# Performance work log

Hardware: AMD Instinct MI355X
Metric: run time of the kernel (lower is better)

The kernel has to match this reference:

```python
import jax, jax.numpy as jnp
import numpy as np

N_NODES = 100000
N_EDGES = 3200000
D = 64          # in == hidden == out channels
EDGE_DIM = 8
N_LAYERS = 3
EPS = 1e-5


def setup_inputs() -> dict:
    key = jax.random.key(0)
    ks = jax.random.split(key, 12)
    x = jax.random.normal(ks[0], (N_NODES, D), dtype=jnp.float32)
    edge_index = jax.random.randint(ks[1], (2, N_EDGES), 0, N_NODES, dtype=jnp.int64)
    edge_attr = jax.random.normal(ks[2], (N_EDGES, EDGE_DIM), dtype=jnp.float32)
    # per-layer HydroConv params (stacked over layers)
    lin_w = jax.random.normal(ks[3], (N_LAYERS, D, D), dtype=jnp.float32) * 0.1
    lin_b = jax.random.normal(ks[4], (N_LAYERS, D), dtype=jnp.float32) * 0.1
    emlp_w = jax.random.normal(ks[5], (N_LAYERS, 1, EDGE_DIM), dtype=jnp.float32) * 0.1
    emlp_b = jax.random.normal(ks[6], (N_LAYERS, 1), dtype=jnp.float32) * 0.1
    # per-layer LayerNorm affine params
    gamma = jnp.ones((N_LAYERS, D), dtype=jnp.float32)
    beta = jnp.zeros((N_LAYERS, D), dtype=jnp.float32)
    fc_w = jax.random.normal(ks[7], (D, D), dtype=jnp.float32) * 0.1
    fc_b = jax.random.normal(ks[8], (D,), dtype=jnp.float32) * 0.1
    return dict(x=x, edge_index=edge_index, edge_attr=edge_attr,
                lin_w=lin_w, lin_b=lin_b, emlp_w=emlp_w, emlp_b=emlp_b,
                gamma=gamma, beta=beta, fc_w=fc_w, fc_b=fc_b)


def _layer_norm(h, g, b):
    mu = jnp.mean(h, axis=-1, keepdims=True)
    var = jnp.var(h, axis=-1, keepdims=True)
    return (h - mu) * jax.lax.rsqrt(var + EPS) * g + b


def reference(x, edge_index, edge_attr, lin_w, lin_b, emlp_w, emlp_b, gamma, beta, fc_w, fc_b):
    src = edge_index[0]  # x_j (source / neighbor)
    dst = edge_index[1]  # x_i (target, aggregation index)
    h = x
    for l in range(N_LAYERS):
        identity = h
        # edge MLP: Linear(edge_dim -> 1) + Softplus  -> per-edge weight [E, 1]
        w = jax.nn.softplus(edge_attr @ emlp_w[l].T + emlp_b[l])
        # message = w * (x_j - x_i); scatter-add to targets
        msg = w * (h[src] - h[dst])                               # [E, D]
        agg = jax.ops.segment_sum(msg, dst, num_segments=N_NODES)  # [N, D]
        h = agg @ lin_w[l].T + lin_b[l]
        h = jax.nn.relu(h)
        h = _layer_norm(h, gamma[l], beta[l])
        h = h + identity  # residual (shapes always match: in == hidden)
    return h @ fc_w.T + fc_b
```

## Files before the change

### kernel.cpp

```cpp
#include <hip/hip_runtime.h>

#define NN 100000
#define NE 3200000
#define NCHUNK 98

__device__ inline unsigned short f2bf(float f) {
    unsigned int u = __float_as_uint(f);
    u += 0x7FFFu + ((u >> 16) & 1u);
    return (unsigned short)(u >> 16);
}
__device__ inline float bflo(unsigned int v) { return __uint_as_float(v << 16); }
__device__ inline float bfhi(unsigned int v) { return __uint_as_float(v & 0xFFFF0000u); }

__global__ __launch_bounds__(256) void k_transpose(
    const float* __restrict__ linw, const float* __restrict__ fcw,
    float* __restrict__ wt)
{
    const float* src = (blockIdx.x < 3) ? (linw + blockIdx.x * 4096) : fcw;
    float* dst = wt + blockIdx.x * 4096;
    for (int i = threadIdx.x; i < 4096; i += 256)
        dst[(i & 63) * 64 + (i >> 6)] = src[i];
}

__global__ __launch_bounds__(256) void k_cvt(
    const float* __restrict__ x, unsigned short* __restrict__ hb)
{
    int stride = gridDim.x * blockDim.x;
    const float4* x4 = (const float4*)x;
    ushort4* hb4 = (ushort4*)hb;
    for (int i = blockIdx.x * blockDim.x + threadIdx.x; i < NN * 16; i += stride) {
        float4 v = x4[i];
        hb4[i] = make_ushort4(f2bf(v.x), f2bf(v.y), f2bf(v.z), f2bf(v.w));
    }
}

__global__ __launch_bounds__(256) void k_hist(
    const int* __restrict__ ei, int* __restrict__ deg)
{
    int stride = gridDim.x * blockDim.x;
    for (int e = blockIdx.x * blockDim.x + threadIdx.x; e < NE; e += stride)
        atomicAdd(&deg[ei[NE + e]], 1);
}

__global__ __launch_bounds__(256) void k_scan1(
    const int* __restrict__ deg, int* __restrict__ base, int* __restrict__ csum)
{
    __shared__ int lds[256];
    int tid = threadIdx.x;
    int i0 = blockIdx.x * 1024 + tid * 4;
    int d[4];
    #pragma unroll
    for (int k = 0; k < 4; ++k) d[k] = (i0 + k < NN) ? deg[i0 + k] : 0;
    int s = d[0] + d[1] + d[2] + d[3];
    lds[tid] = s;
    __syncthreads();
    for (int off = 1; off < 256; off <<= 1) {
        int add = (tid >= off) ? lds[tid - off] : 0;
        __syncthreads();
        lds[tid] += add;
        __syncthreads();
    }
    int excl = lds[tid] - s;
    if (i0 + 0 < NN) base[i0 + 0] = excl;
    if (i0 + 1 < NN) base[i0 + 1] = excl + d[0];
    if (i0 + 2 < NN) base[i0 + 2] = excl + d[0] + d[1];
    if (i0 + 3 < NN) base[i0 + 3] = excl + d[0] + d[1] + d[2];
    if (tid == 255) csum[blockIdx.x] = lds[255];
}

__global__ __launch_bounds__(128) void k_scan2(
    const int* __restrict__ csum, int* __restrict__ coff)
{
    __shared__ int lds[128];
    int tid = threadIdx.x;
    int v = (tid < NCHUNK) ? csum[tid] : 0;
    lds[tid] = v;
    __syncthreads();
    for (int off = 1; off < 128; off <<= 1) {
        int add = (tid >= off) ? lds[tid - off] : 0;
        __syncthreads();
        lds[tid] += add;
        __syncthreads();
    }
    coff[tid] = lds[tid] - v;
}

__global__ __launch_bounds__(256) void k_scan3(
    int* __restrict__ base, int* __restrict__ cursor, const int* __restrict__ coff)
{
    int off = coff[blockIdx.x];
    int i0 = blockIdx.x * 1024 + threadIdx.x * 4;
    #pragma unroll
    for (int k = 0; k < 4; ++k)
        if (i0 + k < NN) {
            int b = base[i0 + k] + off;
            base[i0 + k] = b;
            cursor[i0 + k] = b;
        }
    if (blockIdx.x == 0 && threadIdx.x == 0) base[NN] = NE;
}

__global__ __launch_bounds__(256) void k_fill(
    const int* __restrict__ ei, const float* __restrict__ ea,
    const float* __restrict__ mw, const float* __restrict__ mb,
    int* __restrict__ cursor, uint2* __restrict__ pk)
{
    float wl[3][8], bl[3];
    #pragma unroll
    for (int l = 0; l < 3; ++l) {
        bl[l] = mb[l];
        #pragma unroll
        for (int k = 0; k < 8; ++k) wl[l][k] = mw[l * 8 + k];
    }
    int stride = gridDim.x * blockDim.x;
    const float4* ea4 = (const float4*)ea;
    for (int e = blockIdx.x * blockDim.x + threadIdx.x; e < NE; e += stride) {
        float4 a0 = ea4[2 * e], a1 = ea4[2 * e + 1];
        float av[8] = {a0.x, a0.y, a0.z, a0.w, a1.x, a1.y, a1.z, a1.w};
        unsigned int wb[3];
        #pragma unroll
        for (int l = 0; l < 3; ++l) {
            float xx = bl[l];
            #pragma unroll
            for (int k = 0; k < 8; ++k) xx += av[k] * wl[l][k];
            float sp = fmaxf(xx, 0.f) + log1pf(expf(-fabsf(xx)));
            wb[l] = f2bf(sp) & 0x7FFFu;
        }
        int src = ei[e], dst = ei[NE + e];
        int slot = atomicAdd(&cursor[dst], 1);
        uint2 rec;
        rec.x = (unsigned int)src | (wb[0] << 17);
        rec.y = wb[1] | (wb[2] << 15);
        pk[slot] = rec;
    }
}

template<int L>
__device__ inline float dec_w(uint2 p) {
    if (L == 0) return __uint_as_float((p.x >> 17) << 16);
    if (L == 1) return __uint_as_float((p.y & 0x7FFFu) << 16);
    return __uint_as_float((p.y >> 15) << 16);
}

template<int L>
__global__ __launch_bounds__(256) void k_agg(
    const int* __restrict__ base, const uint2* __restrict__ pk,
    const unsigned short* __restrict__ hb, const float* __restrict__ h,
    float* __restrict__ aout)
{
    int lane = threadIdx.x & 63;
    int sub = lane & 7;
    int g = lane >> 3;
    int wid = (blockIdx.x * blockDim.x + threadIdx.x) >> 6;
    int nwave = (gridDim.x * blockDim.x) >> 6;
    for (int n = wid * 8 + g; n < NN; n += nwave * 8) {
        int s = base[n], e2 = base[n + 1];
        float a0 = 0.f, a1 = 0.f, a2 = 0.f, a3 = 0.f;
        float a4 = 0.f, a5 = 0.f, a6 = 0.f, a7 = 0.f, wsn = 0.f;
        int sl = s;
        for (; sl + 4 <= e2; sl += 4) {
            uint2 p0 = pk[sl], p1 = pk[sl + 1], p2 = pk[sl + 2], p3 = pk[sl + 3];
            uint4 v0 = *(const uint4*)(hb + (((size_t)(p0.x & 0x1FFFF)) << 6) + (sub << 3));
            uint4 v1 = *(const uint4*)(hb + (((size_t)(p1.x & 0x1FFFF)) << 6) + (sub << 3));
            uint4 v2 = *(const uint4*)(hb + (((size_t)(p2.x & 0x1FFFF)) << 6) + (sub << 3));
            uint4 v3 = *(const uint4*)(hb + (((size_t)(p3.x & 0x1FFFF)) << 6) + (sub << 3));
            float w0 = dec_w<L>(p0), w1 = dec_w<L>(p1), w2 = dec_w<L>(p2), w3 = dec_w<L>(p3);
            a0 += w0 * bflo(v0.x); a1 += w0 * bfhi(v0.x); a2 += w0 * bflo(v0.y); a3 += w0 * bfhi(v0.y);
            a4 += w0 * bflo(v0.z); a5 += w0 * bfhi(v0.z); a6 += w0 * bflo(v0.w); a7 += w0 * bfhi(v0.w);
            a0 += w1 * bflo(v1.x); a1 += w1 * bfhi(v1.x); a2 += w1 * bflo(v1.y); a3 += w1 * bfhi(v1.y);
            a4 += w1 * bflo(v1.z); a5 += w1 * bfhi(v1.z); a6 += w1 * bflo(v1.w); a7 += w1 * bfhi(v1.w);
            a0 += w2 * bflo(v2.x); a1 += w2 * bfhi(v2.x); a2 += w2 * bflo(v2.y); a3 += w2 * bfhi(v2.y);
            a4 += w2 * bflo(v2.z); a5 += w2 * bfhi(v2.z); a6 += w2 * bflo(v2.w); a7 += w2 * bfhi(v2.w);
            a0 += w3 * bflo(v3.x); a1 += w3 * bfhi(v3.x); a2 += w3 * bflo(v3.y); a3 += w3 * bfhi(v3.y);
            a4 += w3 * bflo(v3.z); a5 += w3 * bfhi(v3.z); a6 += w3 * bflo(v3.w); a7 += w3 * bfhi(v3.w);
            wsn += w0 + w1 + w2 + w3;
        }
        for (; sl < e2; ++sl) {
            uint2 p = pk[sl];
            uint4 v = *(const uint4*)(hb + (((size_t)(p.x & 0x1FFFF)) << 6) + (sub << 3));
            float w = dec_w<L>(p);
            a0 += w * bflo(v.x); a1 += w * bfhi(v.x); a2 += w * bflo(v.y); a3 += w * bfhi(v.y);
            a4 += w * bflo(v.z); a5 += w * bfhi(v.z); a6 += w * bflo(v.w); a7 += w * bfhi(v.w);
            wsn += w;
        }
        const float* hrow = h + (size_t)n * 64 + sub * 8;
        float4 h0 = *(const float4*)hrow;
        float4 h1 = *(const float4*)(hrow + 4);
        float* orow = aout + (size_t)n * 64 + sub * 8;
        float4 o0 = {a0 - wsn * h0.x, a1 - wsn * h0.y, a2 - wsn * h0.z, a3 - wsn * h0.w};
        float4 o1 = {a4 - wsn * h1.x, a5 - wsn * h1.y, a6 - wsn * h1.z, a7 - wsn * h1.w};
        *(float4*)orow = o0;
        *(float4*)(orow + 4) = o1;
    }
}

__global__ __launch_bounds__(256) void k_node(
    const float* a, const float* __restrict__ hin, float* hout,
    unsigned short* __restrict__ hbout,
    const float* __restrict__ wt, const float* __restrict__ bias,
    const float* __restrict__ gamma, const float* __restrict__ beta)
{
    int n0 = blockIdx.x * blockDim.x + threadIdx.x;
    int stride = gridDim.x * blockDim.x;
    const float4* a4 = (const float4*)a;
    const float4* hin4 = (const float4*)hin;
    float4* ho4 = (float4*)hout;
    ushort4* hb4 = (ushort4*)hbout;
    for (int n = n0; n < NN; n += stride) {
        float y[64];
        #pragma unroll
        for (int j = 0; j < 64; ++j) y[j] = bias[j];
        #pragma unroll 2
        for (int k4 = 0; k4 < 16; ++k4) {
            float4 gg = a4[n * 16 + k4];
            float av[4] = {gg.x, gg.y, gg.z, gg.w};
            #pragma unroll
            for (int kk = 0; kk < 4; ++kk) {
                const float* wr = wt + (k4 * 4 + kk) * 64;
                #pragma unroll
                for (int j = 0; j < 64; ++j) y[j] += av[kk] * wr[j];
            }
        }
        float s = 0.f, s2 = 0.f;
        #pragma unroll
        for (int j = 0; j < 64; ++j) {
            y[j] = fmaxf(y[j], 0.f);
            s += y[j]; s2 += y[j] * y[j];
        }
        float mu = s * (1.f / 64.f);
        float var = s2 * (1.f / 64.f) - mu * mu;
        float inv = rsqrtf(var + 1e-5f);
        #pragma unroll
        for (int j4 = 0; j4 < 16; ++j4) {
            float4 hh = hin4[n * 16 + j4];
            float4 o;
            o.x = (y[4*j4+0] - mu) * inv * gamma[4*j4+0] + beta[4*j4+0] + hh.x;
            o.y = (y[4*j4+1] - mu) * inv * gamma[4*j4+1] + beta[4*j4+1] + hh.y;
            o.z = (y[4*j4+2] - mu) * inv * gamma[4*j4+2] + beta[4*j4+2] + hh.z;
            o.w = (y[4*j4+3] - mu) * inv * gamma[4*j4+3] + beta[4*j4+3] + hh.w;
            ho4[n * 16 + j4] = o;
            if (hbout)
                hb4[n * 16 + j4] = make_ushort4(f2bf(o.x), f2bf(o.y), f2bf(o.z), f2bf(o.w));
        }
    }
}

__global__ __launch_bounds__(256) void k_fc(
    const float* __restrict__ hin, float* __restrict__ out,
    const float* __restrict__ wt, const float* __restrict__ bias)
{
    int n0 = blockIdx.x * blockDim.x + threadIdx.x;
    int stride = gridDim.x * blockDim.x;
    const float4* hin4 = (const float4*)hin;
    float4* o4 = (float4*)out;
    for (int n = n0; n < NN; n += stride) {
        float y[64];
        #pragma unroll
        for (int j = 0; j < 64; ++j) y[j] = bias[j];
        #pragma unroll 2
        for (int k4 = 0; k4 < 16; ++k4) {
            float4 hh = hin4[n * 16 + k4];
            float hv[4] = {hh.x, hh.y, hh.z, hh.w};
            #pragma unroll
            for (int kk = 0; kk < 4; ++kk) {
                const float* wr = wt + (k4 * 4 + kk) * 64;
                #pragma unroll
                for (int j = 0; j < 64; ++j) y[j] += hv[kk] * wr[j];
            }
        }
        #pragma unroll
        for (int j4 = 0; j4 < 16; ++j4) {
            float4 o = {y[4*j4], y[4*j4+1], y[4*j4+2], y[4*j4+3]};
            o4[n * 16 + j4] = o;
        }
    }
}

extern "C" void kernel_launch(void* const* d_in, const int* in_sizes, int n_in,
                              void* d_out, int out_size, void* d_ws, size_t ws_size,
                              hipStream_t stream)
{
    const float* x     = (const float*)d_in[0];
    const int*   ei    = (const int*)d_in[1];
    const float* ea    = (const float*)d_in[2];
    const float* linw  = (const float*)d_in[3];
    const float* linb  = (const float*)d_in[4];
    const float* mw    = (const float*)d_in[5];
    const float* mb    = (const float*)d_in[6];
    const float* gamma = (const float*)d_in[7];
    const float* beta  = (const float*)d_in[8];
    const float* fcw   = (const float*)d_in[9];
    const float* fcb   = (const float*)d_in[10];
    float* out = (float*)d_out;

    float*  A    = (float*)d_ws;
    float*  C    = A + (size_t)NN * 64;
    uint2*  pk   = (uint2*)(C + (size_t)NN * 64);
    unsigned short* hb = (unsigned short*)(pk + NE);
    float*  wt   = (float*)(hb + (size_t)NN * 64);
    int*    deg  = (int*)(wt + 4 * 4096);
    int*    base = deg + NN;
    int*    cur  = base + NN + 1;
    int*    csum = cur + NN;
    int*    coff = csum + 128;

    k_transpose<<<4, 256, 0, stream>>>(linw, fcw, wt);
    k_cvt<<<2048, 256, 0, stream>>>(x, hb);
    hipMemsetAsync(deg, 0, NN * sizeof(int), stream);
    k_hist<<<2048, 256, 0, stream>>>(ei, deg);
    k_scan1<<<NCHUNK, 256, 0, stream>>>(deg, base, csum);
    k_scan2<<<1, 128, 0, stream>>>(csum, coff);
    k_scan3<<<NCHUNK, 256, 0, stream>>>(base, cur, coff);
    k_fill<<<2048, 256, 0, stream>>>(ei, ea, mw, mb, cur, pk);

    k_agg<0><<<3125, 256, 0, stream>>>(base, pk, hb, x, C);
    k_node<<<512, 256, 0, stream>>>(C, x, C, hb, wt + 0 * 4096, linb + 0 * 64,
                                    gamma + 0 * 64, beta + 0 * 64);
    k_agg<1><<<3125, 256, 0, stream>>>(base, pk, hb, C, A);
    k_node<<<512, 256, 0, stream>>>(A, C, A, hb, wt + 1 * 4096, linb + 1 * 64,
                                    gamma + 1 * 64, beta + 1 * 64);
    k_agg<2><<<3125, 256, 0, stream>>>(base, pk, hb, A, C);
    k_node<<<512, 256, 0, stream>>>(C, A, C, (unsigned short*)nullptr,
                                    wt + 2 * 4096, linb + 2 * 64,
                                    gamma + 2 * 64, beta + 2 * 64);

    k_fc<<<512, 256, 0, stream>>>(C, out, wt + 3 * 4096, fcb);
}
```

Measured before the change: 901.9 us.

## Replace global-atomic CSR fill with two-pass bucketed counting sort

CSR construction now runs as a two-level counting sort. Edges are first scattered into 391 coarse buckets of 256 destination nodes, using per-block LDS histograms and an LDS cursor. A second pass then places each edge at its final slot inside its bucket using LDS counters. This replaces the per-edge global atomic cursor and the fully random 8-byte scatter with more localized writes, at the cost of two extra scan passes, one more kernel, and an extra read and write of the staged records. The order of edges within a node becomes nondeterministic, so floating-point summation order may vary between runs.

```diff
diff --git a/kernel.cpp b/kernel.cpp
--- a/kernel.cpp
+++ b/kernel.cpp
@@ -2,7 +2,10 @@
 
 #define NN 100000
 #define NE 3200000
-#define NCHUNK 98
+#define NBKT 391
+#define NBLK 256
+#define EPB (NE / NBLK)
+#define GH_N (NBKT * NBLK)
 
 __device__ inline unsigned short f2bf(float f) {
     unsigned int u = __float_as_uint(f);
@@ -34,23 +37,33 @@
     }
 }
 
-__global__ __launch_bounds__(256) void k_hist(
-    const int* __restrict__ ei, int* __restrict__ deg)
-{
-    int stride = gridDim.x * blockDim.x;
-    for (int e = blockIdx.x * blockDim.x + threadIdx.x; e < NE; e += stride)
-        atomicAdd(&deg[ei[NE + e]], 1);
+__global__ __launch_bounds__(1024) void k_hist2(
+    const int* __restrict__ ei, int* __restrict__ deg, int* __restrict__ gh)
+{
+    __shared__ int lh[NBKT];
+    for (int t = threadIdx.x; t < NBKT; t += 1024) lh[t] = 0;
+    __syncthreads();
+    int bi = blockIdx.x;
+    int e1 = bi * EPB + EPB;
+    for (int e = bi * EPB + threadIdx.x; e < e1; e += 1024) {
+        int dst = ei[NE + e];
+        atomicAdd(&deg[dst], 1);
+        atomicAdd(&lh[dst >> 8], 1);
+    }
+    __syncthreads();
+    for (int t = threadIdx.x; t < NBKT; t += 1024)
+        gh[t * NBLK + bi] = lh[t];
 }
 
 __global__ __launch_bounds__(256) void k_scan1(
-    const int* __restrict__ deg, int* __restrict__ base, int* __restrict__ csum)
+    const int* __restrict__ in, int* __restrict__ out, int* __restrict__ csum, int n)
 {
     __shared__ int lds[256];
     int tid = threadIdx.x;
     int i0 = blockIdx.x * 1024 + tid * 4;
     int d[4];
     #pragma unroll
-    for (int k = 0; k < 4; ++k) d[k] = (i0 + k < NN) ? deg[i0 + k] : 0;
+    for (int k = 0; k < 4; ++k) d[k] = (i0 + k < n) ? in[i0 + k] : 0;
     int s = d[0] + d[1] + d[2] + d[3];
     lds[tid] = s;
     __syncthreads();
@@ -61,19 +74,19 @@
         __syncthreads();
     }
     int excl = lds[tid] - s;
-    if (i0 + 0 < NN) base[i0 + 0] = excl;
-    if (i0 + 1 < NN) base[i0 + 1] = excl + d[0];
-    if (i0 + 2 < NN) base[i0 + 2] = excl + d[0] + d[1];
-    if (i0 + 3 < NN) base[i0 + 3] = excl + d[0] + d[1] + d[2];
+    if (i0 + 0 < n) out[i0 + 0] = excl;
+    if (i0 + 1 < n) out[i0 + 1] = excl + d[0];
+    if (i0 + 2 < n) out[i0 + 2] = excl + d[0] + d[1];
+    if (i0 + 3 < n) out[i0 + 3] = excl + d[0] + d[1] + d[2];
     if (tid == 255) csum[blockIdx.x] = lds[255];
 }
 
 __global__ __launch_bounds__(128) void k_scan2(
-    const int* __restrict__ csum, int* __restrict__ coff)
+    const int* __restrict__ csum, int* __restrict__ coff, int nchunk)
 {
     __shared__ int lds[128];
     int tid = threadIdx.x;
-    int v = (tid < NCHUNK) ? csum[tid] : 0;
+    int v = (tid < nchunk) ? csum[tid] : 0;
     lds[tid] = v;
     __syncthreads();
     for (int off = 1; off < 128; off <<= 1) {
@@ -86,25 +99,26 @@
 }
 
 __global__ __launch_bounds__(256) void k_scan3(
-    int* __restrict__ base, int* __restrict__ cursor, const int* __restrict__ coff)
+    int* __restrict__ arr, const int* __restrict__ coff, int n)
 {
     int off = coff[blockIdx.x];
     int i0 = blockIdx.x * 1024 + threadIdx.x * 4;
     #pragma unroll
     for (int k = 0; k < 4; ++k)
-        if (i0 + k < NN) {
-            int b = base[i0 + k] + off;
-            base[i0 + k] = b;
-            cursor[i0 + k] = b;
-        }
-    if (blockIdx.x == 0 && threadIdx.x == 0) base[NN] = NE;
-}
-
-__global__ __launch_bounds__(256) void k_fill(
+        if (i0 + k < n) arr[i0 + k] += off;
+    if (blockIdx.x == 0 && threadIdx.x == 0) arr[n] = NE;
+}
+
+__global__ __launch_bounds__(1024) void k_fill(
     const int* __restrict__ ei, const float* __restrict__ ea,
     const float* __restrict__ mw, const float* __restrict__ mb,
-    int* __restrict__ cursor, uint2* __restrict__ pk)
-{
+    const int* __restrict__ goff, uint2* __restrict__ stg,
+    unsigned char* __restrict__ stgd)
+{
+    __shared__ int lcur[NBKT];
+    int bi = blockIdx.x;
+    for (int t = threadIdx.x; t < NBKT; t += 1024) lcur[t] = goff[t * NBLK + bi];
+    __syncthreads();
     float wl[3][8], bl[3];
     #pragma unroll
     for (int l = 0; l < 3; ++l) {
@@ -112,9 +126,9 @@
         #pragma unroll
         for (int k = 0; k < 8; ++k) wl[l][k] = mw[l * 8 + k];
     }
-    int stride = gridDim.x * blockDim.x;
     const float4* ea4 = (const float4*)ea;
-    for (int e = blockIdx.x * blockDim.x + threadIdx.x; e < NE; e += stride) {
+    int e1 = bi * EPB + EPB;
+    for (int e = bi * EPB + threadIdx.x; e < e1; e += 1024) {
         float4 a0 = ea4[2 * e], a1 = ea4[2 * e + 1];
         float av[8] = {a0.x, a0.y, a0.z, a0.w, a1.x, a1.y, a1.z, a1.w};
         unsigned int wb[3];
@@ -127,11 +141,34 @@
             wb[l] = f2bf(sp) & 0x7FFFu;
         }
         int src = ei[e], dst = ei[NE + e];
-        int slot = atomicAdd(&cursor[dst], 1);
+        int slot = atomicAdd(&lcur[dst >> 8], 1);
         uint2 rec;
         rec.x = (unsigned int)src | (wb[0] << 17);
         rec.y = wb[1] | (wb[2] << 15);
-        pk[slot] = rec;
+        stg[slot] = rec;
+        stgd[slot] = (unsigned char)(dst & 255);
+    }
+}
+
+__global__ __launch_bounds__(256) void k_fill2(
+    const int* __restrict__ base, const uint2* __restrict__ stg,
+    const unsigned char* __restrict__ stgd, uint2* __restrict__ pk)
+{
+    __shared__ int bl[256];
+    __shared__ int cnt[256];
+    int b = blockIdx.x;
+    int n0 = b * 256;
+    int t = threadIdx.x;
+    if (n0 + t < NN) { bl[t] = base[n0 + t]; }
+    cnt[t] = 0;
+    __syncthreads();
+    int s0 = base[n0];
+    int s1 = (n0 + 256 <= NN) ? base[n0 + 256] : NE;
+    for (int s = s0 + t; s < s1; s += 256) {
+        uint2 rec = stg[s];
+        int dl = stgd[s];
+        int r = atomicAdd(&cnt[dl], 1);
+        pk[bl[dl] + r] = rec;
     }
 }
 
@@ -300,18 +337,25 @@
     float*  wt   = (float*)(hb + (size_t)NN * 64);
     int*    deg  = (int*)(wt + 4 * 4096);
     int*    base = deg + NN;
-    int*    cur  = base + NN + 1;
-    int*    csum = cur + NN;
+    int*    gh   = base + NN + 1;
+    int*    goff = gh + GH_N;
+    int*    csum = goff + GH_N + 1;
     int*    coff = csum + 128;
+    uint2*  stg  = (uint2*)C;
+    unsigned char* stgd = (unsigned char*)A;
 
     k_transpose<<<4, 256, 0, stream>>>(linw, fcw, wt);
     k_cvt<<<2048, 256, 0, stream>>>(x, hb);
     hipMemsetAsync(deg, 0, NN * sizeof(int), stream);
-    k_hist<<<2048, 256, 0, stream>>>(ei, deg);
-    k_scan1<<<NCHUNK, 256, 0, stream>>>(deg, base, csum);
-    k_scan2<<<1, 128, 0, stream>>>(csum, coff);
-    k_scan3<<<NCHUNK, 256, 0, stream>>>(base, cur, coff);
-    k_fill<<<2048, 256, 0, stream>>>(ei, ea, mw, mb, cur, pk);
+    k_hist2<<<NBLK, 1024, 0, stream>>>(ei, deg, gh);
+    k_scan1<<<98, 256, 0, stream>>>(deg, base, csum, NN);
+    k_scan2<<<1, 128, 0, stream>>>(csum, coff, 98);
+    k_scan3<<<98, 256, 0, stream>>>(base, coff, NN);
+    k_scan1<<<98, 256, 0, stream>>>(gh, goff, csum, GH_N);
+    k_scan2<<<1, 128, 0, stream>>>(csum, coff, 98);
+    k_scan3<<<98, 256, 0, stream>>>(goff, coff, GH_N);
+    k_fill<<<NBLK, 1024, 0, stream>>>(ei, ea, mw, mb, goff, stg, stgd);
+    k_fill2<<<NBKT, 256, 0, stream>>>(base, stg, stgd, pk);
 
     k_agg<0><<<3125, 256, 0, stream>>>(base, pk, hb, x, C);
     k_node<<<512, 256, 0, stream>>>(C, x, C, hb, wt + 0 * 4096, linb + 0 * 64,
```

After: 878.4 us. 2.6% less time.
